# Performance work log

Hardware: AMD Instinct MI355X
Metric: run time of the kernel (lower is better)

Reference implementation:

```python
import jax, jax.numpy as jnp
import numpy as np

NUM_HEADS = 16  # from init_kwargs


def setup_inputs() -> dict:
    key = jax.random.key(0)
    k1, k2, k3, k4, k5 = jax.random.split(key, 5)
    B, N, C = 2, 2048, 1024
    return {
        "query": jax.random.normal(k1, (B, N, C), dtype=jnp.float32),
        "key": jax.random.normal(k2, (B, N, C), dtype=jnp.float32),
        "value": jax.random.normal(k3, (B, N, C), dtype=jnp.float32),
        "W_merge": jax.random.normal(k4, (C, C), dtype=jnp.float32) * (1.0 / np.sqrt(C)),
        "b_merge": jax.random.normal(k5, (C,), dtype=jnp.float32) * 0.02,
    }


def reference(query, key, value, W_merge, b_merge):
    B, N, C = query.shape
    H = NUM_HEADS
    dim = C // H
    # Faithful to torch: plain reshape (B,N,C) -> (B, dim, H, N), no transpose.
    q = query.reshape(B, dim, H, -1)
    k = key.reshape(B, dim, H, -1)
    v = value.reshape(B, dim, H, -1)
    # Faithful scale: divide by sqrt(N) (sequence length), as in the source.
    scale = 1.0 / np.sqrt(N).astype(np.float32)
    scores = jnp.einsum('bdhn,bdhm->bhnm', q, k) * scale  # [B,H,N,N]
    attn = jax.nn.softmax(scores, axis=-1)
    x = jnp.einsum('bhnm,bdhm->bdhn', attn, v)  # [B,dim,H,N]
    x = x.reshape(B, C, -1)  # [B,C,N]
    # Conv1d(C,C,kernel_size=1) == pointwise channel matmul + bias
    out = jnp.einsum('oc,bcn->bon', W_merge, x) + b_merge[None, :, None]
    return out  # [B,C,N]
```

## Files before the change

kernel.cpp:

```cpp
#include <hip/hip_runtime.h>


#define H 16
#define NSEQ 2048
#define CCH 1024
#define BATCH 2
#define DSTR (H * NSEQ)

typedef __attribute__((ext_vector_type(8))) short bf16x8;
typedef __attribute__((ext_vector_type(4))) float f32x4;
typedef __attribute__((ext_vector_type(16))) float f32x16;
typedef __attribute__((ext_vector_type(4))) unsigned int uint32x4;

__device__ __forceinline__ unsigned short f2bf(float x) {
  unsigned int u = __builtin_bit_cast(unsigned int, x);
  u += 0x7FFFu + ((u >> 16) & 1u);
  return (unsigned short)(u >> 16);
}

__device__ __forceinline__ unsigned int pack2bf(float a, float b) {
#if __has_builtin(__builtin_amdgcn_cvt_pk_bf16_f32)
  typedef __attribute__((ext_vector_type(2))) __bf16 bf16x2_t;
  bf16x2_t r = __builtin_amdgcn_cvt_pk_bf16_f32(a, b);
  return __builtin_bit_cast(unsigned int, r);
#else
  unsigned int ua = __builtin_bit_cast(unsigned int, a);
  unsigned int ub = __builtin_bit_cast(unsigned int, b);
  ua += 0x7FFFu + ((ua >> 16) & 1u);
  ub += 0x7FFFu + ((ub >> 16) & 1u);
  return __builtin_amdgcn_perm(ub, ua, 0x07060302u);
#endif
}

__device__ __forceinline__ float fast_exp2(float x) {
#if __has_builtin(__builtin_amdgcn_exp2f)
  return __builtin_amdgcn_exp2f(x);
#else
  return exp2f(x);
#endif
}

__device__ __forceinline__ void permswap32(unsigned int& a, unsigned int& b) {
#if __has_builtin(__builtin_amdgcn_permlane32_swap)
  typedef __attribute__((ext_vector_type(2))) unsigned int uint2v;
  uint2v r = __builtin_amdgcn_permlane32_swap(a, b, false, false);
  a = r[0];
  b = r[1];
#else
  unsigned int ax = (unsigned int)__shfl_xor((int)a, 32, 64);
  unsigned int bx = (unsigned int)__shfl_xor((int)b, 32, 64);
  bool lo = (threadIdx.x & 63) < 32;
  unsigned int na = lo ? a : bx;
  unsigned int nb = lo ? ax : b;
  a = na;
  b = nb;
#endif
}

__device__ __forceinline__ void gld16(const void* g, void* l) {
  __builtin_amdgcn_global_load_lds(
      (const __attribute__((address_space(1))) unsigned int*)g,
      (__attribute__((address_space(3))) unsigned int*)l, 16, 0, 0);
}

__device__ __forceinline__ f32x16 zero16() {
  f32x16 v;
#pragma unroll
  for (int i = 0; i < 16; ++i) v[i] = 0.f;
  return v;
}

__global__ __launch_bounds__(256) void prep_all(const float* __restrict__ W,
                                                const float* __restrict__ v,
                                                const float* __restrict__ q,
                                                const float* __restrict__ k,
                                                unsigned short* __restrict__ Wp,
                                                unsigned short* __restrict__ Vb,
                                                unsigned short* __restrict__ Qt,
                                                unsigned short* __restrict__ Kt) {
  __shared__ unsigned short T[64][72];
  const int bid = blockIdx.x, tid = threadIdx.x;

  if (bid < 1024) {
    const int o = bid;
    const int cp = tid * 4;
    const int hh = cp >> 6;
    const int d0 = cp & 63;
    const float* Wr = W + (size_t)o * CCH;
    ushort4 ov;
    ov.x = f2bf(Wr[(d0 + 0) * H + hh]);
    ov.y = f2bf(Wr[(d0 + 1) * H + hh]);
    ov.z = f2bf(Wr[(d0 + 2) * H + hh]);
    ov.w = f2bf(Wr[(d0 + 3) * H + hh]);
    *(ushort4*)&Wp[(size_t)o * CCH + cp] = ov;
  } else if (bid < 5120) {
    int idx = (bid - 1024) * 256 + tid;
    float4 x = ((const float4*)v)[idx];
    ushort4 o;
    o.x = f2bf(x.x); o.y = f2bf(x.y); o.z = f2bf(x.z); o.w = f2bf(x.w);
    ((ushort4*)Vb)[idx] = o;
  } else {
    const int lbid = bid - 5120;
    const int n0 = (lbid & 31) * 64;
    const int hh = (lbid >> 5) & 15;
    const int zz = lbid >> 9;
    const int b = zz >> 1, t = zz & 1;
    const float* src = t ? k : q;
    unsigned short* dst = t ? Kt : Qt;
    const float scl = t ? 1.0f : (0.022097086912079608f * 1.4426950408889634f);
    const size_t base = (size_t)b * (CCH * NSEQ) + (size_t)hh * NSEQ;
#pragma unroll
    for (int it = 0; it < 4; ++it) {
      int i4 = it * 256 + tid;
      int d = i4 >> 4;
      int nn = (i4 & 15) << 2;
      float4 val = *(const float4*)(src + base + (size_t)d * DSTR + n0 + nn);
      T[nn + 0][d] = f2bf(val.x * scl);
      T[nn + 1][d] = f2bf(val.y * scl);
      T[nn + 2][d] = f2bf(val.z * scl);
      T[nn + 3][d] = f2bf(val.w * scl);
    }
    __syncthreads();
    const size_t obase = ((size_t)(b * H + hh) * NSEQ + n0) * 64;
#pragma unroll
    for (int it = 0; it < 2; ++it) {
      int idx = it * 256 + tid;
      int row = idx >> 3, cb = idx & 7;
      *(bf16x8*)(dst + obase + (size_t)row * 64 + cb * 8) = *(const bf16x8*)&T[row][cb * 8];
    }
  }
}

__global__ __launch_bounds__(512, 4) void attn6(const unsigned short* __restrict__ Qt,
                                                const unsigned short* __restrict__ Kt,
                                                const unsigned short* __restrict__ Vb,
                                                unsigned short* __restrict__ xt) {
  __shared__ __align__(16) unsigned char sbuf[65536 + 1024];
  unsigned short* KV = (unsigned short*)sbuf;
  float* lsumLDS = (float*)(sbuf + 65536);
  float* Oex = (float*)sbuf;

  const int tid = threadIdx.x;
  const int w = tid >> 6, lane = tid & 63;
  const int lane31 = lane & 31, hl = lane >> 5;
  const int g = w >> 2, nw = w & 3;
  const int n0 = blockIdx.x * 128;
  const int hh = blockIdx.y, b = blockIdx.z;

  const unsigned short* Qbase = Qt + ((size_t)(b * H + hh) * NSEQ + n0) * 64;
  const unsigned short* Kg = Kt + ((size_t)(b * H + hh) * NSEQ + g * 1024) * 64;
  const unsigned short* Vg = Vb + (size_t)b * (CCH * NSEQ) + (size_t)hh * NSEQ + g * 1024;

  const int r8 = lane >> 3, scb = lane & 7;

#define KVOFF(gg, bb, kk) ((((gg)*2 + (bb)) * 2 + (kk)) * 4096)

#pragma unroll
  for (int i = 0; i < 2; ++i) {
    int row = i * 64 + w * 8 + r8;
    int cbl = scb ^ (row & 7);
    gld16(Qbase + (size_t)row * 64 + cbl * 8, KV + (i * 64 + w * 8) * 64);
  }
  __syncthreads();

  bf16x8 bQ[4];
#pragma unroll
  for (int ks = 0; ks < 4; ++ks) {
    int row = nw * 32 + lane31;
    int phys = (ks * 2 + hl) ^ (row & 7);
    bQ[ks] = *(const bf16x8*)(KV + (size_t)row * 64 + phys * 8);
  }
  __syncthreads();

#pragma unroll
  for (int i = 0; i < 2; ++i) {
    int row = i * 32 + nw * 8 + r8;
    int cbl = scb ^ (row & 7);
    gld16(Kg + (size_t)row * 64 + cbl * 8, KV + KVOFF(g, 0, 0) + (i * 32 + nw * 8) * 64);
    gld16(Vg + (size_t)row * DSTR + cbl * 8, KV + KVOFF(g, 0, 1) + (i * 32 + nw * 8) * 64);
  }
  __syncthreads();

  f32x16 O[2];
  O[0] = zero16();
  O[1] = zero16();
  float lsum = 0.f;

  for (int it = 0; it < 16; ++it) {
    const int cur = it & 1;
    if (it < 15) {
      const int nxt = cur ^ 1;
      const int m0n = (it + 1) * 64;
#pragma unroll
      for (int i = 0; i < 2; ++i) {
        int row = i * 32 + nw * 8 + r8;
        int cbl = scb ^ (row & 7);
        gld16(Kg + (size_t)(m0n + row) * 64 + cbl * 8,
              KV + KVOFF(g, nxt, 0) + (i * 32 + nw * 8) * 64);
        gld16(Vg + (size_t)row * DSTR + m0n + cbl * 8,
              KV + KVOFF(g, nxt, 1) + (i * 32 + nw * 8) * 64);
      }
    }

#pragma unroll
    for (int mt = 0; mt < 2; ++mt) {
      f32x16 St = zero16();
#pragma unroll
      for (int ks = 0; ks < 4; ++ks) {
        int row = mt * 32 + lane31;
        int phys = (ks * 2 + hl) ^ (row & 7);
        bf16x8 aK = *(const bf16x8*)(KV + KVOFF(g, cur, 0) + row * 64 + phys * 8);
        St = __builtin_amdgcn_mfma_f32_32x32x16_bf16(aK, bQ[ks], St, 0, 0, 0);
      }

      unsigned int pd[8];
#pragma unroll
      for (int t = 0; t < 8; ++t) {
        float e0 = fast_exp2(St[2 * t]);
        float e1 = fast_exp2(St[2 * t + 1]);
        lsum += e0 + e1;
        pd[t] = pack2bf(e0, e1);
      }

      unsigned int s0[4] = {pd[0], pd[1], pd[2], pd[3]};
      unsigned int s1[4] = {pd[4], pd[5], pd[6], pd[7]};
      permswap32(s0[0], s0[2]);
      permswap32(s0[1], s0[3]);
      permswap32(s1[0], s1[2]);
      permswap32(s1[1], s1[3]);

#pragma unroll
      for (int ms = 0; ms < 2; ++ms) {
        bf16x8 bV[2];
#pragma unroll
        for (int dt = 0; dt < 2; ++dt) {
          int row = dt * 32 + lane31;
          int phys = (mt * 4 + ms * 2 + hl) ^ (row & 7);
          bV[dt] = *(const bf16x8*)(KV + KVOFF(g, cur, 1) + row * 64 + phys * 8);
        }
        const unsigned int* sp = ms ? s1 : s0;
        bf16x8 aP = __builtin_bit_cast(bf16x8, (uint32x4){sp[0], sp[1], sp[2], sp[3]});
        O[0] = __builtin_amdgcn_mfma_f32_32x32x16_bf16(aP, bV[0], O[0], 0, 0, 0);
        O[1] = __builtin_amdgcn_mfma_f32_32x32x16_bf16(aP, bV[1], O[1], 0, 0, 0);
      }
    }
    __syncthreads();
  }

  lsum += __shfl_xor(lsum, 32, 64);
  if (hl == 0) lsumLDS[g * 128 + nw * 32 + lane31] = lsum;
  if (g == 1) {
#pragma unroll
    for (int dt = 0; dt < 2; ++dt)
#pragma unroll
      for (int r = 0; r < 16; ++r) {
        int nl = nw * 32 + (r & 3) + 8 * (r >> 2) + 4 * hl;
        Oex[nl * 64 + dt * 32 + lane31] = O[dt][r];
      }
  }
  __syncthreads();
  if (g == 0) {
    const size_t xb = (size_t)b * ((size_t)NSEQ * CCH);
#pragma unroll
    for (int rq = 0; rq < 4; ++rq) {
      int nlb = nw * 32 + rq * 8 + 4 * hl;
      float4 l0 = *(const float4*)&lsumLDS[nlb];
      float4 l1 = *(const float4*)&lsumLDS[128 + nlb];
      float inv0 = 1.0f / (l0.x + l1.x);
      float inv1 = 1.0f / (l0.y + l1.y);
      float inv2 = 1.0f / (l0.z + l1.z);
      float inv3 = 1.0f / (l0.w + l1.w);
#pragma unroll
      for (int dt = 0; dt < 2; ++dt) {
        int d = dt * 32 + lane31;
#pragma unroll
        for (int rr = 0; rr < 4; ++rr) {
          int r = rq * 4 + rr;
          float val = O[dt][r] + Oex[(nlb + rr) * 64 + d];
          float inv = (rr == 0) ? inv0 : (rr == 1) ? inv1 : (rr == 2) ? inv2 : inv3;
          int n = n0 + nlb + rr;
          xt[xb + (size_t)n * CCH + hh * 64 + d] = f2bf(val * inv);
        }
      }
    }
  }
#undef KVOFF
}

__global__ __launch_bounds__(256) void merge5(const unsigned short* __restrict__ Wp,
                                              const unsigned short* __restrict__ xt,
                                              const float* __restrict__ bias,
                                              float* __restrict__ out) {
  __shared__ unsigned short At[2][64 * 64];
  __shared__ unsigned short Bt[2][64 * 64];
  const int tid = threadIdx.x;
  const int w = tid >> 6, lane = tid & 63;
  const int quad = lane >> 4, l16 = lane & 15;
  const int wx = w & 1, wy = w >> 1;
  const int n0 = blockIdx.x * 64, o0 = blockIdx.y * 64, b = blockIdx.z;
  const int srow = w * 8 + (lane >> 3), scb = lane & 7;
  const unsigned short* Bbase = xt + (size_t)b * ((size_t)NSEQ * CCH);

  f32x4 acc[2][2];
#pragma unroll
  for (int ot = 0; ot < 2; ++ot)
#pragma unroll
    for (int nt = 0; nt < 2; ++nt) acc[ot][nt] = (f32x4){0.f, 0.f, 0.f, 0.f};

#pragma unroll
  for (int i = 0; i < 2; ++i) {
    int row = i * 32 + srow;
    int cbl = scb ^ (row & 7);
    gld16(Wp + (size_t)(o0 + row) * CCH + cbl * 8, &At[0][(i * 32 + w * 8) * 64]);
    gld16(Bbase + (size_t)(n0 + row) * CCH + cbl * 8, &Bt[0][(i * 32 + w * 8) * 64]);
  }
  __syncthreads();

  for (int it = 0; it < 16; ++it) {
    const int cur = it & 1;
    if (it < 15) {
      const int nxt = cur ^ 1;
      const int c0 = (it + 1) * 64;
#pragma unroll
      for (int i = 0; i < 2; ++i) {
        int row = i * 32 + srow;
        int cbl = scb ^ (row & 7);
        gld16(Wp + (size_t)(o0 + row) * CCH + c0 + cbl * 8, &At[nxt][(i * 32 + w * 8) * 64]);
        gld16(Bbase + (size_t)(n0 + row) * CCH + c0 + cbl * 8, &Bt[nxt][(i * 32 + w * 8) * 64]);
      }
    }
#pragma unroll
    for (int ks = 0; ks < 2; ++ks) {
      int phys = ((ks * 4 + quad) ^ (l16 & 7)) * 8;
      bf16x8 aW[2], bX[2];
#pragma unroll
      for (int ot = 0; ot < 2; ++ot)
        aW[ot] = *(const bf16x8*)&At[cur][(wy * 32 + ot * 16 + l16) * 64 + phys];
#pragma unroll
      for (int nt = 0; nt < 2; ++nt)
        bX[nt] = *(const bf16x8*)&Bt[cur][(wx * 32 + nt * 16 + l16) * 64 + phys];
#pragma unroll
      for (int ot = 0; ot < 2; ++ot)
#pragma unroll
        for (int nt = 0; nt < 2; ++nt)
          acc[ot][nt] =
              __builtin_amdgcn_mfma_f32_16x16x32_bf16(aW[ot], bX[nt], acc[ot][nt], 0, 0, 0);
    }
    __syncthreads();
  }

#pragma unroll
  for (int ot = 0; ot < 2; ++ot) {
#pragma unroll
    for (int r = 0; r < 4; ++r) {
      int o = o0 + wy * 32 + ot * 16 + quad * 4 + r;
      float br = bias[o];
#pragma unroll
      for (int nt = 0; nt < 2; ++nt)
        out[(size_t)b * ((size_t)CCH * NSEQ) + (size_t)o * NSEQ + n0 + wx * 32 + nt * 16 + l16] =
            acc[ot][nt][r] + br;
    }
  }
}

extern "C" void kernel_launch(void* const* d_in, const int* in_sizes, int n_in,
                              void* d_out, int out_size, void* d_ws, size_t ws_size,
                              hipStream_t stream) {
  const float* q = (const float*)d_in[0];
  const float* k = (const float*)d_in[1];
  const float* v = (const float*)d_in[2];
  const float* W = (const float*)d_in[3];
  const float* bias = (const float*)d_in[4];
  float* out = (float*)d_out;

  unsigned short* Wp = (unsigned short*)d_ws;
  unsigned short* xt = Wp + (1u << 20);
  unsigned short* Qt = xt + (4u << 20);
  unsigned short* Kt = Qt + (4u << 20);
  unsigned short* Vb = Kt + (4u << 20);

  hipLaunchKernelGGL(prep_all, dim3(7168), dim3(256), 0, stream, W, v, q, k, Wp, Vb, Qt, Kt);
  hipLaunchKernelGGL(attn6, dim3(NSEQ / 128, H, BATCH), dim3(512), 0, stream, Qt, Kt, Vb, xt);
  hipLaunchKernelGGL(merge5, dim3(NSEQ / 64, CCH / 64, BATCH), dim3(256), 0, stream,
                     Wp, xt, bias, out);
}
```

Baseline: 160.3 us.

## Fuse Q bf16 conversion into attention kernel and stage W permute through LDS

Q conversion, scaling and transposition move from the prep kernel into the attention kernel, which loads raw fp32 Q and writes the swizzled bf16 tile straight to LDS. This removes the Qt workspace round trip and 1024 prep blocks. The W permute in prep now does coalesced float4 loads into shared memory instead of strided scalar global reads. The cost is extra fp32 load and conversion work at the start of each attention block, which is read once per block.

New measurement: 161.9 us. No clear change (+1.0%).

```diff
diff --git a/kernel.cpp b/kernel.cpp
--- a/kernel.cpp
+++ b/kernel.cpp
@@ -72,27 +72,29 @@
 
 __global__ __launch_bounds__(256) void prep_all(const float* __restrict__ W,
                                                 const float* __restrict__ v,
-                                                const float* __restrict__ q,
                                                 const float* __restrict__ k,
                                                 unsigned short* __restrict__ Wp,
                                                 unsigned short* __restrict__ Vb,
-                                                unsigned short* __restrict__ Qt,
                                                 unsigned short* __restrict__ Kt) {
   __shared__ unsigned short T[64][72];
   const int bid = blockIdx.x, tid = threadIdx.x;
 
   if (bid < 1024) {
+    unsigned short* WT = &T[0][0];
     const int o = bid;
-    const int cp = tid * 4;
-    const int hh = cp >> 6;
-    const int d0 = cp & 63;
-    const float* Wr = W + (size_t)o * CCH;
+    float4 wv = ((const float4*)(W + (size_t)o * CCH))[tid];
+    WT[tid * 4 + 0] = f2bf(wv.x);
+    WT[tid * 4 + 1] = f2bf(wv.y);
+    WT[tid * 4 + 2] = f2bf(wv.z);
+    WT[tid * 4 + 3] = f2bf(wv.w);
+    __syncthreads();
+    const int cp0 = tid * 4;
     ushort4 ov;
-    ov.x = f2bf(Wr[(d0 + 0) * H + hh]);
-    ov.y = f2bf(Wr[(d0 + 1) * H + hh]);
-    ov.z = f2bf(Wr[(d0 + 2) * H + hh]);
-    ov.w = f2bf(Wr[(d0 + 3) * H + hh]);
-    *(ushort4*)&Wp[(size_t)o * CCH + cp] = ov;
+    ov.x = WT[((cp0 + 0) & 63) * 16 + ((cp0 + 0) >> 6)];
+    ov.y = WT[((cp0 + 1) & 63) * 16 + ((cp0 + 1) >> 6)];
+    ov.z = WT[((cp0 + 2) & 63) * 16 + ((cp0 + 2) >> 6)];
+    ov.w = WT[((cp0 + 3) & 63) * 16 + ((cp0 + 3) >> 6)];
+    *(ushort4*)&Wp[(size_t)o * CCH + cp0] = ov;
   } else if (bid < 5120) {
     int idx = (bid - 1024) * 256 + tid;
     float4 x = ((const float4*)v)[idx];
@@ -103,22 +105,18 @@
     const int lbid = bid - 5120;
     const int n0 = (lbid & 31) * 64;
     const int hh = (lbid >> 5) & 15;
-    const int zz = lbid >> 9;
-    const int b = zz >> 1, t = zz & 1;
-    const float* src = t ? k : q;
-    unsigned short* dst = t ? Kt : Qt;
-    const float scl = t ? 1.0f : (0.022097086912079608f * 1.4426950408889634f);
+    const int b = lbid >> 9;
     const size_t base = (size_t)b * (CCH * NSEQ) + (size_t)hh * NSEQ;
 #pragma unroll
     for (int it = 0; it < 4; ++it) {
       int i4 = it * 256 + tid;
       int d = i4 >> 4;
       int nn = (i4 & 15) << 2;
-      float4 val = *(const float4*)(src + base + (size_t)d * DSTR + n0 + nn);
-      T[nn + 0][d] = f2bf(val.x * scl);
-      T[nn + 1][d] = f2bf(val.y * scl);
-      T[nn + 2][d] = f2bf(val.z * scl);
-      T[nn + 3][d] = f2bf(val.w * scl);
+      float4 val = *(const float4*)(k + base + (size_t)d * DSTR + n0 + nn);
+      T[nn + 0][d] = f2bf(val.x);
+      T[nn + 1][d] = f2bf(val.y);
+      T[nn + 2][d] = f2bf(val.z);
+      T[nn + 3][d] = f2bf(val.w);
     }
     __syncthreads();
     const size_t obase = ((size_t)(b * H + hh) * NSEQ + n0) * 64;
@@ -126,12 +124,12 @@
     for (int it = 0; it < 2; ++it) {
       int idx = it * 256 + tid;
       int row = idx >> 3, cb = idx & 7;
-      *(bf16x8*)(dst + obase + (size_t)row * 64 + cb * 8) = *(const bf16x8*)&T[row][cb * 8];
-    }
-  }
-}
-
-__global__ __launch_bounds__(512, 4) void attn6(const unsigned short* __restrict__ Qt,
+      *(bf16x8*)(Kt + obase + (size_t)row * 64 + cb * 8) = *(const bf16x8*)&T[row][cb * 8];
+    }
+  }
+}
+
+__global__ __launch_bounds__(512, 4) void attn8(const float* __restrict__ q,
                                                 const unsigned short* __restrict__ Kt,
                                                 const unsigned short* __restrict__ Vb,
                                                 unsigned short* __restrict__ xt) {
@@ -139,6 +137,7 @@
   unsigned short* KV = (unsigned short*)sbuf;
   float* lsumLDS = (float*)(sbuf + 65536);
   float* Oex = (float*)sbuf;
+  unsigned short* Qs = KV;
 
   const int tid = threadIdx.x;
   const int w = tid >> 6, lane = tid & 63;
@@ -147,7 +146,7 @@
   const int n0 = blockIdx.x * 128;
   const int hh = blockIdx.y, b = blockIdx.z;
 
-  const unsigned short* Qbase = Qt + ((size_t)(b * H + hh) * NSEQ + n0) * 64;
+  const float* Qraw = q + (size_t)b * (CCH * NSEQ) + (size_t)hh * NSEQ;
   const unsigned short* Kg = Kt + ((size_t)(b * H + hh) * NSEQ + g * 1024) * 64;
   const unsigned short* Vg = Vb + (size_t)b * (CCH * NSEQ) + (size_t)hh * NSEQ + g * 1024;
 
@@ -155,11 +154,20 @@
 
 #define KVOFF(gg, bb, kk) ((((gg)*2 + (bb)) * 2 + (kk)) * 4096)
 
-#pragma unroll
-  for (int i = 0; i < 2; ++i) {
-    int row = i * 64 + w * 8 + r8;
-    int cbl = scb ^ (row & 7);
-    gld16(Qbase + (size_t)row * 64 + cbl * 8, KV + (i * 64 + w * 8) * 64);
+  const float qscl = 0.022097086912079608f * 1.4426950408889634f;
+#pragma unroll
+  for (int it2 = 0; it2 < 4; ++it2) {
+    int i4 = it2 * 512 + tid;
+    int d = i4 >> 5;
+    int nn = (i4 & 31) << 2;
+    float4 val = *(const float4*)(Qraw + (size_t)d * DSTR + n0 + nn);
+    int ch = d >> 3, di = d & 7;
+#pragma unroll
+    for (int j = 0; j < 4; ++j) {
+      float x = (j == 0) ? val.x : (j == 1) ? val.y : (j == 2) ? val.z : val.w;
+      int n = nn + j;
+      Qs[n * 64 + ((ch ^ (n & 7)) * 8 + di)] = f2bf(x * qscl);
+    }
   }
   __syncthreads();
 
@@ -375,12 +383,11 @@
 
   unsigned short* Wp = (unsigned short*)d_ws;
   unsigned short* xt = Wp + (1u << 20);
-  unsigned short* Qt = xt + (4u << 20);
-  unsigned short* Kt = Qt + (4u << 20);
+  unsigned short* Kt = xt + (4u << 20);
   unsigned short* Vb = Kt + (4u << 20);
 
-  hipLaunchKernelGGL(prep_all, dim3(7168), dim3(256), 0, stream, W, v, q, k, Wp, Vb, Qt, Kt);
-  hipLaunchKernelGGL(attn6, dim3(NSEQ / 128, H, BATCH), dim3(512), 0, stream, Qt, Kt, Vb, xt);
+  hipLaunchKernelGGL(prep_all, dim3(6144), dim3(256), 0, stream, W, v, k, Wp, Vb, Kt);
+  hipLaunchKernelGGL(attn8, dim3(NSEQ / 128, H, BATCH), dim3(512), 0, stream, q, Kt, Vb, xt);
   hipLaunchKernelGGL(merge5, dim3(NSEQ / 64, CCH / 64, BATCH), dim3(256), 0, stream,
                      Wp, xt, bias, out);
 }
```

## Store K/V tiles in LDS in MFMA fragment order and stage W transpose through LDS

Applied to the files above, without the earlier changes.

The attention kernel now has each lane load K and V into LDS already laid out in the order the MFMA operands are read, so reads become a plain lane-contiguous index with no XOR swizzle math, and the global pointers simply advance each iteration. The softmax row sum is accumulated with a bf16 dot2 against ones on the packed probabilities, replacing the two float adds. The W-permute prep stage now does a coalesced float4 load, then transposes through LDS instead of using strided global gathers. Risks are LDS bank conflicts in the new layout, less coalesced global K/V access, and the row sum now being built from bf16-rounded values.

Measured after the change: 164.6 us. 2.7% more time.

```diff
diff --git a/kernel.cpp b/kernel.cpp
--- a/kernel.cpp
+++ b/kernel.cpp
@@ -29,6 +29,17 @@
   ua += 0x7FFFu + ((ua >> 16) & 1u);
   ub += 0x7FFFu + ((ub >> 16) & 1u);
   return __builtin_amdgcn_perm(ub, ua, 0x07060302u);
+#endif
+}
+
+__device__ __forceinline__ float sum2bf(unsigned int pk, float acc, float e0, float e1) {
+#if __has_builtin(__builtin_amdgcn_fdot2_f32_bf16)
+  typedef __attribute__((ext_vector_type(2))) __bf16 bf16x2_t;
+  const unsigned int ones_u = 0x3F803F80u;
+  return __builtin_amdgcn_fdot2_f32_bf16(__builtin_bit_cast(bf16x2_t, pk),
+                                         __builtin_bit_cast(bf16x2_t, ones_u), acc, false);
+#else
+  return acc + e0 + e1;
 #endif
 }
 
@@ -82,17 +93,21 @@
   const int bid = blockIdx.x, tid = threadIdx.x;
 
   if (bid < 1024) {
+    unsigned short* WT = &T[0][0];
     const int o = bid;
-    const int cp = tid * 4;
-    const int hh = cp >> 6;
-    const int d0 = cp & 63;
-    const float* Wr = W + (size_t)o * CCH;
+    float4 wv = ((const float4*)(W + (size_t)o * CCH))[tid];
+    WT[tid * 4 + 0] = f2bf(wv.x);
+    WT[tid * 4 + 1] = f2bf(wv.y);
+    WT[tid * 4 + 2] = f2bf(wv.z);
+    WT[tid * 4 + 3] = f2bf(wv.w);
+    __syncthreads();
+    const int cp0 = tid * 4;
     ushort4 ov;
-    ov.x = f2bf(Wr[(d0 + 0) * H + hh]);
-    ov.y = f2bf(Wr[(d0 + 1) * H + hh]);
-    ov.z = f2bf(Wr[(d0 + 2) * H + hh]);
-    ov.w = f2bf(Wr[(d0 + 3) * H + hh]);
-    *(ushort4*)&Wp[(size_t)o * CCH + cp] = ov;
+    ov.x = WT[((cp0 + 0) & 63) * 16 + ((cp0 + 0) >> 6)];
+    ov.y = WT[((cp0 + 1) & 63) * 16 + ((cp0 + 1) >> 6)];
+    ov.z = WT[((cp0 + 2) & 63) * 16 + ((cp0 + 2) >> 6)];
+    ov.w = WT[((cp0 + 3) & 63) * 16 + ((cp0 + 3) >> 6)];
+    *(ushort4*)&Wp[(size_t)o * CCH + cp0] = ov;
   } else if (bid < 5120) {
     int idx = (bid - 1024) * 256 + tid;
     float4 x = ((const float4*)v)[idx];
@@ -131,7 +146,7 @@
   }
 }
 
-__global__ __launch_bounds__(512, 4) void attn6(const unsigned short* __restrict__ Qt,
+__global__ __launch_bounds__(512, 4) void attn9(const unsigned short* __restrict__ Qt,
                                                 const unsigned short* __restrict__ Kt,
                                                 const unsigned short* __restrict__ Vb,
                                                 unsigned short* __restrict__ xt) {
@@ -172,13 +187,19 @@
   }
   __syncthreads();
 
-#pragma unroll
-  for (int i = 0; i < 2; ++i) {
-    int row = i * 32 + nw * 8 + r8;
-    int cbl = scb ^ (row & 7);
-    gld16(Kg + (size_t)row * 64 + cbl * 8, KV + KVOFF(g, 0, 0) + (i * 32 + nw * 8) * 64);
-    gld16(Vg + (size_t)row * DSTR + cbl * 8, KV + KVOFF(g, 0, 1) + (i * 32 + nw * 8) * 64);
-  }
+  const unsigned short* kp0 = Kg + (size_t)(0 * 32 + lane31) * 64 + nw * 16 + hl * 8;
+  const unsigned short* kp1 = Kg + (size_t)(1 * 32 + lane31) * 64 + nw * 16 + hl * 8;
+  const int idx0 = nw, idx1 = 4 + nw;
+  const unsigned short* vp0 =
+      Vg + (size_t)((idx0 >> 2) * 32 + lane31) * DSTR + ((idx0 >> 1) & 1) * 32 + (idx0 & 1) * 16 + hl * 8;
+  const unsigned short* vp1 =
+      Vg + (size_t)((idx1 >> 2) * 32 + lane31) * DSTR + ((idx1 >> 1) & 1) * 32 + (idx1 & 1) * 16 + hl * 8;
+
+  gld16(kp0, KV + KVOFF(g, 0, 0) + (0 * 4 + nw) * 512);
+  gld16(kp1, KV + KVOFF(g, 0, 0) + (1 * 4 + nw) * 512);
+  gld16(vp0, KV + KVOFF(g, 0, 1) + idx0 * 512);
+  gld16(vp1, KV + KVOFF(g, 0, 1) + idx1 * 512);
+  kp0 += 64 * 64; kp1 += 64 * 64; vp0 += 64; vp1 += 64;
   __syncthreads();
 
   f32x16 O[2];
@@ -190,16 +211,11 @@
     const int cur = it & 1;
     if (it < 15) {
       const int nxt = cur ^ 1;
-      const int m0n = (it + 1) * 64;
-#pragma unroll
-      for (int i = 0; i < 2; ++i) {
-        int row = i * 32 + nw * 8 + r8;
-        int cbl = scb ^ (row & 7);
-        gld16(Kg + (size_t)(m0n + row) * 64 + cbl * 8,
-              KV + KVOFF(g, nxt, 0) + (i * 32 + nw * 8) * 64);
-        gld16(Vg + (size_t)row * DSTR + m0n + cbl * 8,
-              KV + KVOFF(g, nxt, 1) + (i * 32 + nw * 8) * 64);
-      }
+      gld16(kp0, KV + KVOFF(g, nxt, 0) + (0 * 4 + nw) * 512);
+      gld16(kp1, KV + KVOFF(g, nxt, 0) + (1 * 4 + nw) * 512);
+      gld16(vp0, KV + KVOFF(g, nxt, 1) + idx0 * 512);
+      gld16(vp1, KV + KVOFF(g, nxt, 1) + idx1 * 512);
+      kp0 += 64 * 64; kp1 += 64 * 64; vp0 += 64; vp1 += 64;
     }
 
 #pragma unroll
@@ -207,9 +223,7 @@
       f32x16 St = zero16();
 #pragma unroll
       for (int ks = 0; ks < 4; ++ks) {
-        int row = mt * 32 + lane31;
-        int phys = (ks * 2 + hl) ^ (row & 7);
-        bf16x8 aK = *(const bf16x8*)(KV + KVOFF(g, cur, 0) + row * 64 + phys * 8);
+        bf16x8 aK = *(const bf16x8*)(KV + KVOFF(g, cur, 0) + ((mt * 4 + ks) * 64 + lane) * 8);
         St = __builtin_amdgcn_mfma_f32_32x32x16_bf16(aK, bQ[ks], St, 0, 0, 0);
       }
 
@@ -218,8 +232,8 @@
       for (int t = 0; t < 8; ++t) {
         float e0 = fast_exp2(St[2 * t]);
         float e1 = fast_exp2(St[2 * t + 1]);
-        lsum += e0 + e1;
         pd[t] = pack2bf(e0, e1);
+        lsum = sum2bf(pd[t], lsum, e0, e1);
       }
 
       unsigned int s0[4] = {pd[0], pd[1], pd[2], pd[3]};
@@ -233,11 +247,9 @@
       for (int ms = 0; ms < 2; ++ms) {
         bf16x8 bV[2];
 #pragma unroll
-        for (int dt = 0; dt < 2; ++dt) {
-          int row = dt * 32 + lane31;
-          int phys = (mt * 4 + ms * 2 + hl) ^ (row & 7);
-          bV[dt] = *(const bf16x8*)(KV + KVOFF(g, cur, 1) + row * 64 + phys * 8);
-        }
+        for (int dt = 0; dt < 2; ++dt)
+          bV[dt] = *(const bf16x8*)(KV + KVOFF(g, cur, 1) +
+                                    (((dt * 2 + mt) * 2 + ms) * 64 + lane) * 8);
         const unsigned int* sp = ms ? s1 : s0;
         bf16x8 aP = __builtin_bit_cast(bf16x8, (uint32x4){sp[0], sp[1], sp[2], sp[3]});
         O[0] = __builtin_amdgcn_mfma_f32_32x32x16_bf16(aP, bV[0], O[0], 0, 0, 0);
@@ -380,7 +392,7 @@
   unsigned short* Vb = Kt + (4u << 20);
 
   hipLaunchKernelGGL(prep_all, dim3(7168), dim3(256), 0, stream, W, v, q, k, Wp, Vb, Qt, Kt);
-  hipLaunchKernelGGL(attn6, dim3(NSEQ / 128, H, BATCH), dim3(512), 0, stream, Qt, Kt, Vb, xt);
+  hipLaunchKernelGGL(attn9, dim3(NSEQ / 128, H, BATCH), dim3(512), 0, stream, Qt, Kt, Vb, xt);
   hipLaunchKernelGGL(merge5, dim3(NSEQ / 64, CCH / 64, BATCH), dim3(256), 0, stream,
                      Wp, xt, bias, out);
 }
```
